# Performance work log

Hardware: AMD Instinct MI355X
Metric: run time of the kernel (lower is better)

Reference implementation:

```python
import jax, jax.numpy as jnp
import numpy as np

ALPHA = 3.5
BETA = 0.5
GAMMA = 0.5
LAM = 0.5


def setup_inputs() -> dict:
    key = jax.random.key(0)
    k1, k2 = jax.random.split(key)
    b, c, t = 32, 512, 4096
    x = jax.random.normal(k1, (b, c, t), dtype=jnp.float32)
    # original: z0 ~ U[0.25, 0.75]
    z0 = jax.random.uniform(k2, (b, c), dtype=jnp.float32) * 0.5 + 0.25
    return {"x": x, "z0": z0}


def reference(x, z0):
    # x: (b, c, t), z0: (b, c)
    x_t_first = jnp.transpose(x, (2, 0, 1))  # (t, b, c)

    def step(z, x_t):
        sigma_in = ALPHA * z * (1.0 - z) + BETA * x_t
        z_next = (1.0 - GAMMA) * z + GAMMA * 0.5 * (1.0 + jnp.tanh(sigma_in))
        z_next = jnp.clip(z_next, 0.0, 1.0)
        u_t = LAM * x_t + (1.0 - LAM) * (2.0 * z_next - 1.0)
        return z_next, u_t

    _, u = jax.lax.scan(step, z0, x_t_first)  # u: (t, b, c)
    return jnp.transpose(u, (1, 2, 0))  # (b, c, t)
```

## Files before the change

kernel.cpp:

```cpp
#include <hip/hip_runtime.h>


#define SEQ_T 4096
#define PF 8
#define NBLK (SEQ_T / (PF * 4))

__device__ __forceinline__ void chaos_step(float& z, float xs, float& us) {
    const float CA = -10.098865286222744f;
    const float CB = -1.4426950408889634f;
    float p  = CB * xs;
    float hz = 0.5f * z;
    float zz = __builtin_fmaf(-z, z, z);
    float s  = __builtin_fmaf(CA, zz, p);
    float e  = exp2f(s);
    float r  = __builtin_amdgcn_rcpf(e + 1.0f);
    z = __builtin_fmaf(0.5f, r, hz);
    us = __builtin_fmaf(0.5f, xs, z - 0.5f);
}

__global__ __launch_bounds__(64, 1)
void ChaosModulator_28922309771717_kernel(const float* __restrict__ x,
                                          const float* __restrict__ z0,
                                          float* __restrict__ u) {
    const int seq = blockIdx.x * 64 + threadIdx.x;
    const float4* __restrict__ xv = (const float4*)(x + (size_t)seq * SEQ_T);
    float4* __restrict__ uv = (float4*)(u + (size_t)seq * SEQ_T);

    float z = z0[seq];

    float4 buf[PF];
#pragma unroll
    for (int k = 0; k < PF; ++k) buf[k] = xv[k];

    for (int blk = 0; blk < NBLK; ++blk) {
        float4 cur[PF];
#pragma unroll
        for (int k = 0; k < PF; ++k) cur[k] = buf[k];

        if (blk + 1 < NBLK) {
#pragma unroll
            for (int k = 0; k < PF; ++k) buf[k] = xv[(blk + 1) * PF + k];
        }

#pragma unroll
        for (int k = 0; k < PF; ++k) {
            float4 xq = cur[k];
            float4 uq;
            chaos_step(z, xq.x, uq.x);
            chaos_step(z, xq.y, uq.y);
            chaos_step(z, xq.z, uq.z);
            chaos_step(z, xq.w, uq.w);
            uv[blk * PF + k] = uq;
        }
    }
}

extern "C" void kernel_launch(void* const* d_in, const int* in_sizes, int n_in,
                              void* d_out, int out_size, void* d_ws, size_t ws_size,
                              hipStream_t stream) {
    const float* x  = (const float*)d_in[0];
    const float* z0 = (const float*)d_in[1];
    float* u = (float*)d_out;

    const int n_seq = in_sizes[1];
    dim3 grid(n_seq / 64), block(64);
    ChaosModulator_28922309771717_kernel<<<grid, block, 0, stream>>>(x, z0, u);
}
```

Before: 527.4 us.

## Stage time tiles through swizzled LDS for coalesced global loads and stores

Before, each thread read and wrote its own row with float4 accesses that sat 16 KB apart across lanes, so global accesses were uncoalesced. Now the 64-row block loads 128-step tiles cooperatively (two rows per wavefront access, 32 lanes contiguous) into XOR-swizzled shared memory. Each thread runs its recurrence out of LDS and writes results back in place, and the tile is then stored coalesced. It also swaps exp2f for the hardware exp2 intrinsic. The cost is two barriers per tile and 32 float4 prefetch registers.

```diff
diff --git a/kernel.cpp b/kernel.cpp
--- a/kernel.cpp
+++ b/kernel.cpp
@@ -2,8 +2,10 @@
 
 
 #define SEQ_T 4096
-#define PF 8
-#define NBLK (SEQ_T / (PF * 4))
+#define TT    128
+#define NT    (SEQ_T / TT)
+#define NG    (TT / 4)
+#define ROWS  64
 
 __device__ __forceinline__ void chaos_step(float& z, float xs, float& us) {
     const float CA = -10.098865286222744f;
@@ -12,9 +14,9 @@
     float hz = 0.5f * z;
     float zz = __builtin_fmaf(-z, z, z);
     float s  = __builtin_fmaf(CA, zz, p);
-    float e  = exp2f(s);
+    float e  = __builtin_amdgcn_exp2f(s);
     float r  = __builtin_amdgcn_rcpf(e + 1.0f);
-    z = __builtin_fmaf(0.5f, r, hz);
+    z  = __builtin_fmaf(0.5f, r, hz);
     us = __builtin_fmaf(0.5f, xs, z - 0.5f);
 }
 
@@ -22,35 +24,60 @@
 void ChaosModulator_28922309771717_kernel(const float* __restrict__ x,
                                           const float* __restrict__ z0,
                                           float* __restrict__ u) {
-    const int seq = blockIdx.x * 64 + threadIdx.x;
-    const float4* __restrict__ xv = (const float4*)(x + (size_t)seq * SEQ_T);
-    float4* __restrict__ uv = (float4*)(u + (size_t)seq * SEQ_T);
+    __shared__ __align__(16) float lds[ROWS * TT];
 
-    float z = z0[seq];
+    const int L = threadIdx.x;
+    const int seqbase = blockIdx.x * ROWS;
+    const int rhi = L >> 5;
+    const int gw  = L & 31;
+    const int sw  = L & 7;
 
-    float4 buf[PF];
+    const float* __restrict__ xb = x + (size_t)seqbase * SEQ_T;
+    float* __restrict__ ub       = u + (size_t)seqbase * SEQ_T;
+
+    float4 pf[NG];
 #pragma unroll
-    for (int k = 0; k < PF; ++k) buf[k] = xv[k];
+    for (int i = 0; i < NG; ++i) {
+        int r = 2 * i + rhi;
+        pf[i] = *(const float4*)(xb + (size_t)r * SEQ_T + gw * 4);
+    }
 
-    for (int blk = 0; blk < NBLK; ++blk) {
-        float4 cur[PF];
+    float z = z0[seqbase + L];
+
+    for (int k = 0; k < NT; ++k) {
 #pragma unroll
-        for (int k = 0; k < PF; ++k) cur[k] = buf[k];
+        for (int i = 0; i < NG; ++i) {
+            int r = 2 * i + rhi;
+            *(float4*)&lds[r * TT + ((gw ^ (r & 7)) << 2)] = pf[i];
+        }
+        __syncthreads();
 
-        if (blk + 1 < NBLK) {
+        if (k + 1 < NT) {
 #pragma unroll
-            for (int k = 0; k < PF; ++k) buf[k] = xv[(blk + 1) * PF + k];
+            for (int i = 0; i < NG; ++i) {
+                int r = 2 * i + rhi;
+                pf[i] = *(const float4*)(xb + (size_t)r * SEQ_T + (k + 1) * TT + gw * 4);
+            }
         }
 
 #pragma unroll
-        for (int k = 0; k < PF; ++k) {
-            float4 xq = cur[k];
+        for (int g = 0; g < NG; ++g) {
+            float* p = &lds[L * TT + ((g ^ sw) << 2)];
+            float4 xq = *(float4*)p;
             float4 uq;
             chaos_step(z, xq.x, uq.x);
             chaos_step(z, xq.y, uq.y);
             chaos_step(z, xq.z, uq.z);
             chaos_step(z, xq.w, uq.w);
-            uv[blk * PF + k] = uq;
+            *(float4*)p = uq;
+        }
+        __syncthreads();
+
+#pragma unroll
+        for (int i = 0; i < NG; ++i) {
+            int r = 2 * i + rhi;
+            float4 uq = *(const float4*)&lds[r * TT + ((gw ^ (r & 7)) << 2)];
+            *(float4*)(ub + (size_t)r * SEQ_T + k * TT + gw * 4) = uq;
         }
     }
 }
@@ -60,9 +87,9 @@
                               hipStream_t stream) {
     const float* x  = (const float*)d_in[0];
     const float* z0 = (const float*)d_in[1];
-    float* u = (float*)d_out;
+    float* uo = (float*)d_out;
 
     const int n_seq = in_sizes[1];
-    dim3 grid(n_seq / 64), block(64);
-    ChaosModulator_28922309771717_kernel<<<grid, block, 0, stream>>>(x, z0, u);
+    dim3 grid(n_seq / ROWS), block(ROWS);
+    ChaosModulator_28922309771717_kernel<<<grid, block, 0, stream>>>(x, z0, uo);
 }
```

After: 541.0 us. +2.6%, slower.
